# Optimization experiments

Hardware: AMD Instinct MI355X
Metric: run time of the kernel (lower is better)

The kernel has to match this reference:

```python
import jax, jax.numpy as jnp
import numpy as np


def setup_inputs() -> dict:
    key = jax.random.key(0)
    f = jax.random.normal(key, (8, 96, 256, 256), dtype=jnp.float32)
    return {"f": f}


def reference(f):
    # Reshape (B, 96, H, W) -> (B, C=12, D=8, H, W) as in the original module.
    B, _, H, W = f.shape
    C, D = 12, 8
    x = f.reshape(B, C, D, H, W)
    # Original: for each voxel, sum of squared diffs to every voxel in its
    # clamped (truncated at boundaries) 3x3x3 neighborhood. Equivalent to
    # summing, over each of the 27 shifts, (center - shifted)^2 on the
    # overlapping region (out-of-bounds pairs are simply excluded).
    loss = jnp.float32(0.0)
    for dk in (-1, 0, 1):
        for di in (-1, 0, 1):
            for dj in (-1, 0, 1):
                a = x[:, :,
                      max(0, -dk):D - max(0, dk),
                      max(0, -di):H - max(0, di),
                      max(0, -dj):W - max(0, dj)]
                b = x[:, :,
                      max(0, dk):D - max(0, -dk),
                      max(0, di):H - max(0, -di),
                      max(0, dj):W - max(0, -dj)]
                loss = loss + jnp.sum((a - b) ** 2)
    return loss
```

## Files before the change

### kernel.cpp

```cpp
#include <hip/hip_runtime.h>


constexpr int WIDTH  = 256;
constexpr int HWs    = 256 * 256;
constexpr int NBLOCK = 8 * 12 * 256 / 4;

__global__ __launch_bounds__(256, 2) void lap3d(const float* __restrict__ f,
                                                float* __restrict__ partial) {
    const int tid  = threadIdx.x;
    const int lane = tid & 63;
    const int wid  = tid >> 6;
    const int row  = blockIdx.x * 4 + wid;
    const int i    = row & 255;
    const int bc   = row >> 8;
    const float* base = f + (size_t)bc * 8 * HWs + (size_t)i * WIDTH + (size_t)lane * 4;

    const bool has_down  = (i < 255);
    const bool has_right = (lane < 63);
    const bool has_left  = (lane > 0);

    float o[8][4], nx[8][4];
#pragma unroll
    for (int k = 0; k < 8; ++k) {
        float4 v = *reinterpret_cast<const float4*>(base + k * HWs);
        o[k][0] = v.x; o[k][1] = v.y; o[k][2] = v.z; o[k][3] = v.w;
    }
    if (has_down) {
#pragma unroll
        for (int k = 0; k < 8; ++k) {
            float4 v = *reinterpret_cast<const float4*>(base + k * HWs + WIDTH);
            nx[k][0] = v.x; nx[k][1] = v.y; nx[k][2] = v.z; nx[k][3] = v.w;
        }
    } else {
#pragma unroll
        for (int k = 0; k < 8; ++k) { nx[k][0] = nx[k][1] = nx[k][2] = nx[k][3] = 0.f; }
    }

    float eo[8], nl[8], nr[8];
#pragma unroll
    for (int k = 0; k < 8; ++k) {
        eo[k] = __shfl_down(o[k][0], 1);
        nr[k] = __shfl_down(nx[k][0], 1);
        nl[k] = __shfl_up(nx[k][3], 1);
    }

    float acc = 0.f;

#pragma unroll
    for (int k = 0; k < 7; ++k)
#pragma unroll
        for (int m = 0; m < 4; ++m) { float d = o[k][m] - o[k + 1][m]; acc += d * d; }

#pragma unroll
    for (int k = 0; k < 8; ++k)
#pragma unroll
        for (int dk = -1; dk <= 1; ++dk) {
            const int kk = k + dk;
            if (kk < 0 || kk > 7) continue;
#pragma unroll
            for (int m = 0; m < 3; ++m) { float d = o[k][m] - o[kk][m + 1]; acc += d * d; }
            if (has_right) { float d = o[k][3] - eo[kk]; acc += d * d; }
        }

    if (has_down) {
#pragma unroll
        for (int k = 0; k < 8; ++k)
#pragma unroll
            for (int dk = -1; dk <= 1; ++dk) {
                const int kk = k + dk;
                if (kk < 0 || kk > 7) continue;
#pragma unroll
                for (int m = 0; m < 4; ++m) { float d = o[k][m] - nx[kk][m]; acc += d * d; }
#pragma unroll
                for (int m = 0; m < 3; ++m) { float d = o[k][m] - nx[kk][m + 1]; acc += d * d; }
                if (has_right) { float d = o[k][3] - nr[kk]; acc += d * d; }
#pragma unroll
                for (int m = 1; m < 4; ++m) { float d = o[k][m] - nx[kk][m - 1]; acc += d * d; }
                if (has_left) { float d = o[k][0] - nl[kk]; acc += d * d; }
            }
    }

#pragma unroll
    for (int off = 32; off > 0; off >>= 1) acc += __shfl_down(acc, off);

    __shared__ float wsum[4];
    if (lane == 0) wsum[wid] = acc;
    __syncthreads();
    if (tid == 0) partial[blockIdx.x] = wsum[0] + wsum[1] + wsum[2] + wsum[3];
}

__global__ __launch_bounds__(256) void lap3d_reduce(const float* __restrict__ partial,
                                                    float* __restrict__ out) {
    float s = 0.f;
    for (int i = threadIdx.x; i < NBLOCK; i += 256) s += partial[i];
#pragma unroll
    for (int off = 32; off > 0; off >>= 1) s += __shfl_down(s, off);
    __shared__ float w[4];
    if ((threadIdx.x & 63) == 0) w[threadIdx.x >> 6] = s;
    __syncthreads();
    if (threadIdx.x == 0) out[0] = 2.0f * (w[0] + w[1] + w[2] + w[3]);
}

extern "C" void kernel_launch(void* const* d_in, const int* in_sizes, int n_in,
                              void* d_out, int out_size, void* d_ws, size_t ws_size,
                              hipStream_t stream) {
    const float* f = (const float*)d_in[0];
    float* partial = (float*)d_ws;
    float* out = (float*)d_out;
    lap3d<<<dim3(NBLOCK), dim3(256), 0, stream>>>(f, partial);
    lap3d_reduce<<<dim3(1), dim3(256), 0, stream>>>(partial, out);
}
```

Before: 272.3 us.

## Process four consecutive rows per wave, reusing the loaded row as next center

Each wavefront now walks a strip of four consecutive H rows and carries the loaded next row forward as the new center row. Each input row is then fetched about once plus a one-row halo per strip, instead of twice as before. The block count drops by four, and launch bounds are raised to 4 waves per SIMD, which caps registers while each thread holds two 8x4 register tiles. The longer serial per-thread loop and the register pressure could limit latency hiding.

```diff
diff --git a/kernel.cpp b/kernel.cpp
--- a/kernel.cpp
+++ b/kernel.cpp
@@ -3,66 +3,53 @@
 
 constexpr int WIDTH  = 256;
 constexpr int HWs    = 256 * 256;
-constexpr int NBLOCK = 8 * 12 * 256 / 4;
+constexpr int NSTRIP = 8 * 12 * 256 / 4;
+constexpr int NBLOCK = NSTRIP / 4;
 
-__global__ __launch_bounds__(256, 2) void lap3d(const float* __restrict__ f,
+__global__ __launch_bounds__(256, 4) void lap3d(const float* __restrict__ f,
                                                 float* __restrict__ partial) {
     const int tid  = threadIdx.x;
     const int lane = tid & 63;
     const int wid  = tid >> 6;
-    const int row  = blockIdx.x * 4 + wid;
-    const int i    = row & 255;
-    const int bc   = row >> 8;
-    const float* base = f + (size_t)bc * 8 * HWs + (size_t)i * WIDTH + (size_t)lane * 4;
+    const int ss   = blockIdx.x * 4 + wid;
+    const int bc   = ss >> 6;
+    const int i0   = (ss & 63) << 2;
+    const float* base = f + (size_t)bc * 8 * HWs + (size_t)i0 * WIDTH + (size_t)lane * 4;
 
-    const bool has_down  = (i < 255);
-    const bool has_right = (lane < 63);
-    const bool has_left  = (lane > 0);
+    const bool has_right  = (lane < 63);
+    const bool has_left   = (lane > 0);
+    const bool last_strip = (i0 == 252);
 
-    float o[8][4], nx[8][4];
+    float cur[8][4];
 #pragma unroll
     for (int k = 0; k < 8; ++k) {
         float4 v = *reinterpret_cast<const float4*>(base + k * HWs);
-        o[k][0] = v.x; o[k][1] = v.y; o[k][2] = v.z; o[k][3] = v.w;
-    }
-    if (has_down) {
-#pragma unroll
-        for (int k = 0; k < 8; ++k) {
-            float4 v = *reinterpret_cast<const float4*>(base + k * HWs + WIDTH);
-            nx[k][0] = v.x; nx[k][1] = v.y; nx[k][2] = v.z; nx[k][3] = v.w;
-        }
-    } else {
-#pragma unroll
-        for (int k = 0; k < 8; ++k) { nx[k][0] = nx[k][1] = nx[k][2] = nx[k][3] = 0.f; }
-    }
-
-    float eo[8], nl[8], nr[8];
-#pragma unroll
-    for (int k = 0; k < 8; ++k) {
-        eo[k] = __shfl_down(o[k][0], 1);
-        nr[k] = __shfl_down(nx[k][0], 1);
-        nl[k] = __shfl_up(nx[k][3], 1);
+        cur[k][0] = v.x; cur[k][1] = v.y; cur[k][2] = v.z; cur[k][3] = v.w;
     }
 
     float acc = 0.f;
 
 #pragma unroll
-    for (int k = 0; k < 7; ++k)
+    for (int s = 0; s < 4; ++s) {
+        const bool hn = (s < 3) || !last_strip;
+        float nxt[8][4];
+        if (hn) {
+            const float* nb = base + (s + 1) * WIDTH;
 #pragma unroll
-        for (int m = 0; m < 4; ++m) { float d = o[k][m] - o[k + 1][m]; acc += d * d; }
+            for (int k = 0; k < 8; ++k) {
+                float4 v = *reinterpret_cast<const float4*>(nb + k * HWs);
+                nxt[k][0] = v.x; nxt[k][1] = v.y; nxt[k][2] = v.z; nxt[k][3] = v.w;
+            }
+        }
 
 #pragma unroll
-    for (int k = 0; k < 8; ++k)
+        for (int k = 0; k < 7; ++k)
 #pragma unroll
-        for (int dk = -1; dk <= 1; ++dk) {
-            const int kk = k + dk;
-            if (kk < 0 || kk > 7) continue;
+            for (int m = 0; m < 4; ++m) { float d = cur[k][m] - cur[k + 1][m]; acc += d * d; }
+
+        float eo[8];
 #pragma unroll
-            for (int m = 0; m < 3; ++m) { float d = o[k][m] - o[kk][m + 1]; acc += d * d; }
-            if (has_right) { float d = o[k][3] - eo[kk]; acc += d * d; }
-        }
-
-    if (has_down) {
+        for (int k = 0; k < 8; ++k) eo[k] = __shfl_down(cur[k][0], 1);
 #pragma unroll
         for (int k = 0; k < 8; ++k)
 #pragma unroll
@@ -70,14 +57,37 @@
                 const int kk = k + dk;
                 if (kk < 0 || kk > 7) continue;
 #pragma unroll
-                for (int m = 0; m < 4; ++m) { float d = o[k][m] - nx[kk][m]; acc += d * d; }
+                for (int m = 0; m < 3; ++m) { float d = cur[k][m] - cur[kk][m + 1]; acc += d * d; }
+                if (has_right) { float d = cur[k][3] - eo[kk]; acc += d * d; }
+            }
+
+        if (hn) {
+            float nr[8], nl[8];
 #pragma unroll
-                for (int m = 0; m < 3; ++m) { float d = o[k][m] - nx[kk][m + 1]; acc += d * d; }
-                if (has_right) { float d = o[k][3] - nr[kk]; acc += d * d; }
+            for (int k = 0; k < 8; ++k) {
+                nr[k] = __shfl_down(nxt[k][0], 1);
+                nl[k] = __shfl_up(nxt[k][3], 1);
+            }
 #pragma unroll
-                for (int m = 1; m < 4; ++m) { float d = o[k][m] - nx[kk][m - 1]; acc += d * d; }
-                if (has_left) { float d = o[k][0] - nl[kk]; acc += d * d; }
-            }
+            for (int k = 0; k < 8; ++k)
+#pragma unroll
+                for (int dk = -1; dk <= 1; ++dk) {
+                    const int kk = k + dk;
+                    if (kk < 0 || kk > 7) continue;
+#pragma unroll
+                    for (int m = 0; m < 4; ++m) { float d = cur[k][m] - nxt[kk][m]; acc += d * d; }
+#pragma unroll
+                    for (int m = 0; m < 3; ++m) { float d = cur[k][m] - nxt[kk][m + 1]; acc += d * d; }
+                    if (has_right) { float d = cur[k][3] - nr[kk]; acc += d * d; }
+#pragma unroll
+                    for (int m = 1; m < 4; ++m) { float d = cur[k][m] - nxt[kk][m - 1]; acc += d * d; }
+                    if (has_left) { float d = cur[k][0] - nl[kk]; acc += d * d; }
+                }
+#pragma unroll
+            for (int k = 0; k < 8; ++k)
+#pragma unroll
+                for (int m = 0; m < 4; ++m) cur[k][m] = nxt[k][m];
+        }
     }
 
 #pragma unroll
```

Result: slower. 372.2 us (+36.7%).
